# Optimization experiments

Measured on AMD Instinct MI355X. Metric: run time of the kernel, lower is better.

The kernel has to match this reference:

```python
import jax, jax.numpy as jnp
import numpy as np

INPUT_DIM = 256
NODE_DIM = 6
OUTPUT_DIM = 256
N_NODES = 10000
N_EDGES = 320000


def setup_inputs() -> dict:
    key = jax.random.key(0)
    ks = jax.random.split(key, 6)
    x = jax.random.normal(ks[0], (N_NODES, NODE_DIM), dtype=jnp.float32)
    edge_index = jax.random.randint(ks[1], (2, N_EDGES), 0, N_NODES, dtype=jnp.int64 if jax.config.jax_enable_x64 else jnp.int32)
    edge_attr = jax.random.normal(ks[2], (N_EDGES, INPUT_DIM), dtype=jnp.float32)
    mask = jax.random.uniform(ks[3], (N_EDGES,), dtype=jnp.float32)
    in_feat = INPUT_DIM * 3 + NODE_DIM * 2  # 774
    limit = float(np.sqrt(6.0 / (in_feat + OUTPUT_DIM)))  # xavier_uniform
    W = jax.random.uniform(ks[4], (OUTPUT_DIM, in_feat), dtype=jnp.float32, minval=-limit, maxval=limit)
    b = jax.random.uniform(ks[5], (OUTPUT_DIM,), dtype=jnp.float32, minval=-1.0 / np.sqrt(in_feat), maxval=1.0 / np.sqrt(in_feat))
    return {"x": x, "num_nodes": N_NODES, "edge_index": edge_index, "edge_attr": edge_attr, "mask": mask, "W": W, "b": b}


def reference(x, num_nodes, edge_index, edge_attr, mask, W, b):
    row = edge_index[0]
    col = edge_index[1]
    # masked mean-ish aggregation of edge features into destination nodes
    num = jax.ops.segment_sum(edge_attr * mask[:, None], col, num_segments=num_nodes)  # [N, input_dim]
    den = jax.ops.segment_sum(mask[:, None], col, num_segments=num_nodes)             # [N, 1]
    node_rep = num / (den + 1.0)
    node_rep = jnp.concatenate([node_rep, x], axis=1)  # [N, input_dim + node_dim]
    edge_rep = jnp.concatenate([node_rep[row], node_rep[col], edge_attr], axis=-1)  # [E, 3*input_dim + 2*node_dim]
    edge_rep = edge_rep @ W.T + b  # [E, output_dim]
    return (node_rep, edge_rep)
```

## Files before the change

### kernel.cpp

```cpp
#include <hip/hip_runtime.h>
#include <hip/hip_bf16.h>
#include <stdint.h>

typedef __attribute__((ext_vector_type(4))) float f32x4;
typedef __attribute__((ext_vector_type(8))) short bf16x8;

#define NDIM 6
#define IN_DIM 256
#define OUT_DIM 256
#define KW 780
#define NR 262
#define NRP 320
#define SCAN_T 1024

__device__ __forceinline__ short f2bf(float f) {
  return __builtin_bit_cast(short, __float2bfloat16(f));
}
__device__ __forceinline__ float bf2f(short h) {
  unsigned int u = ((unsigned int)(unsigned short)h) << 16;
  return __builtin_bit_cast(float, u);
}

__device__ __forceinline__ void gload_lds16(void* lds, const void* g) {
  __builtin_amdgcn_global_load_lds(
      (const __attribute__((address_space(1))) unsigned int*)g,
      (__attribute__((address_space(3))) unsigned int*)lds, 16, 0, 0);
}

__global__ void hist_kernel(const int* __restrict__ ei, int* __restrict__ counts, int E) {
  int e = blockIdx.x * 256 + threadIdx.x;
  if (e < E) atomicAdd(&counts[ei[(long)E + e]], 1);
}

__global__ __launch_bounds__(SCAN_T) void scan_kernel(const int* __restrict__ counts,
                                                      int* __restrict__ offsets, int N) {
  __shared__ int part[SCAN_T];
  int t = threadIdx.x;
  int chunk = (N + SCAN_T - 1) / SCAN_T;
  int begin = t * chunk;
  int s = 0;
  for (int i = 0; i < chunk; ++i) {
    int idx = begin + i;
    if (idx < N) s += counts[idx];
  }
  part[t] = s;
  __syncthreads();
  for (int d = 1; d < SCAN_T; d <<= 1) {
    int v = (t >= d) ? part[t - d] : 0;
    __syncthreads();
    part[t] += v;
    __syncthreads();
  }
  int run = (t == 0) ? 0 : part[t - 1];
  for (int i = 0; i < chunk; ++i) {
    int idx = begin + i;
    if (idx < N) { offsets[idx] = run; run += counts[idx]; }
  }
}

__global__ void scatter_kernel(const int* __restrict__ ei, const int* __restrict__ offsets,
                               int* __restrict__ cursor, int* __restrict__ csr, int E) {
  int e = blockIdx.x * 256 + threadIdx.x;
  if (e >= E) return;
  int col = ei[(long)E + e];
  int pos = atomicAdd(&cursor[col], 1);
  csr[offsets[col] + pos] = e;
}

__global__ __launch_bounds__(256) void reduce_kernel(
    const int* __restrict__ csr, const int* __restrict__ offsets,
    const int* __restrict__ counts, const float* __restrict__ ea,
    const float* __restrict__ mask, const float* __restrict__ x,
    float* __restrict__ outN, short* __restrict__ nrepb, int N) {
  int n = blockIdx.x * 4 + (threadIdx.x >> 6);
  if (n >= N) return;
  int lane = threadIdx.x & 63;
  int s = offsets[n], cnt = counts[n];
  f32x4 sum = (f32x4)0.0f;
  float den = 0.0f;

  int ecur = 0; float mcur = 0.0f;
  if (lane < cnt) { ecur = csr[s + lane]; mcur = mask[ecur]; }

  for (int base = 0; base < cnt; base += 64) {
    int enext = 0; float mnext = 0.0f;
    if (base + 64 < cnt) {
      int idx = base + 64 + lane;
      if (idx < cnt) { enext = csr[s + idx]; mnext = mask[enext]; }
    }
    int mbits = __builtin_bit_cast(int, mcur);
#pragma unroll
    for (int i = 0; i < 64; ++i) {
      if (base + i >= cnt) break;
      int e = __builtin_amdgcn_readlane(ecur, i);
      float m = __builtin_bit_cast(float, __builtin_amdgcn_readlane(mbits, i));
      f32x4 v = ((const f32x4*)ea)[(long)e * 64 + lane];
      sum.x += v.x * m; sum.y += v.y * m; sum.z += v.z * m; sum.w += v.w * m;
      den += m;
    }
    ecur = enext; mcur = mnext;
  }

  float inv = 1.0f / (den + 1.0f);
  sum.x *= inv; sum.y *= inv; sum.z *= inv; sum.w *= inv;
  float* po = outN + (long)n * NR + lane * 4;
  po[0] = sum.x; po[1] = sum.y; po[2] = sum.z; po[3] = sum.w;
  short4 pb;
  pb.x = f2bf(sum.x); pb.y = f2bf(sum.y); pb.z = f2bf(sum.z); pb.w = f2bf(sum.w);
  *(short4*)(nrepb + (long)n * NRP + lane * 4) = pb;
  if (lane < NDIM) {
    float xv = x[(long)n * NDIM + lane];
    outN[(long)n * NR + IN_DIM + lane] = xv;
    nrepb[(long)n * NRP + IN_DIM + lane] = f2bf(xv);
  } else if (lane < 8) {
    nrepb[(long)n * NRP + IN_DIM + lane] = 0;
  }
}

__global__ void wprep_kernel(const float* __restrict__ W, short* __restrict__ Weat,
                             short* __restrict__ Wrt, short* __restrict__ Wct) {
  int idx = blockIdx.x * 256 + threadIdx.x;
  if (idx < OUT_DIM * 256) {
    int n = idx >> 8, k = idx & 255;
    Weat[idx] = f2bf(W[(long)n * KW + 2 * NR + k]);
    return;
  }
  idx -= OUT_DIM * 256;
  if (idx < OUT_DIM * NRP) {
    int n = idx / NRP, k = idx % NRP;
    Wrt[idx] = f2bf(k < NR ? W[(long)n * KW + k] : 0.0f);
    return;
  }
  idx -= OUT_DIM * NRP;
  if (idx < OUT_DIM * NRP) {
    int n = idx / NRP, k = idx % NRP;
    Wct[idx] = f2bf(k < NR ? W[(long)n * KW + NR + k] : 0.0f);
  }
}

__global__ __launch_bounds__(256, 2) void pgemm_kernel(
    const short* __restrict__ nrepb, const short* __restrict__ Wrt,
    const short* __restrict__ Wct, const float* __restrict__ bias,
    short* __restrict__ Pr, short* __restrict__ Pc, int N) {
  __shared__ short As[5][64 * 64];
  const int tid = threadIdx.x;
  const int wave = tid >> 6, lane = tid & 63;
  const int m0 = blockIdx.x * 64;
  const int table = blockIdx.y;
  const short* Wt = table ? Wct : Wrt;
  short* P = table ? Pc : Pr;
  const int nbase = wave * 64;

  float bvals[4];
#pragma unroll
  for (int nf = 0; nf < 4; ++nf)
    bvals[nf] = table ? 0.0f : bias[nbase + 16 * nf + (lane & 15)];

  f32x4 acc[4][4];
#pragma unroll
  for (int mf = 0; mf < 4; ++mf)
#pragma unroll
    for (int nf = 0; nf < 4; ++nf) acc[mf][nf] = (f32x4)0.0f;

  bf16x8 bv[2][8];
  auto loadB = [&](int t, int tb) {
#pragma unroll
    for (int s2 = 0; s2 < 2; ++s2)
#pragma unroll
      for (int nf = 0; nf < 4; ++nf)
        bv[tb][s2 * 4 + nf] = *(const bf16x8*)&Wt[
            (long)(nbase + nf * 16 + (lane & 15)) * NRP + t * 64 + s2 * 32 + (lane >> 4) * 8];
  };

  const int scp = lane & 7;
#pragma unroll
  for (int t = 0; t < 5; ++t)
#pragma unroll
    for (int i = 0; i < 2; ++i) {
      int row = 16 * wave + 8 * i + (lane >> 3);
      int c = scp ^ (row & 7);
      long m = m0 + row; if (m >= N) m = N - 1;
      gload_lds16(&As[t][(16 * wave + 8 * i) * 64], nrepb + m * NRP + t * 64 + 8 * c);
    }
  loadB(0, 0);
  asm volatile("s_waitcnt vmcnt(8)" ::: "memory");
  __builtin_amdgcn_s_barrier();
  __builtin_amdgcn_sched_barrier(0);

#pragma unroll
  for (int t = 0; t < 5; ++t) {
    if (t < 4) loadB(t + 1, (t + 1) & 1);
    if (t < 4) asm volatile("s_waitcnt vmcnt(8)" ::: "memory");
    else       asm volatile("s_waitcnt vmcnt(0)" ::: "memory");
#pragma unroll
    for (int s2 = 0; s2 < 2; ++s2) {
      bf16x8 a[4];
      int cl = s2 * 4 + (lane >> 4);
#pragma unroll
      for (int mf = 0; mf < 4; ++mf) {
        int m = 16 * mf + (lane & 15);
        a[mf] = *(const bf16x8*)&As[t][m * 64 + ((cl ^ (m & 7)) * 8)];
      }
#pragma unroll
      for (int mf = 0; mf < 4; ++mf)
#pragma unroll
        for (int nf = 0; nf < 4; ++nf)
          acc[mf][nf] = __builtin_amdgcn_mfma_f32_16x16x32_bf16(
              a[mf], bv[t & 1][s2 * 4 + nf], acc[mf][nf], 0, 0, 0);
    }
  }

#pragma unroll
  for (int mf = 0; mf < 4; ++mf)
#pragma unroll
    for (int nf = 0; nf < 4; ++nf)
#pragma unroll
      for (int q = 0; q < 4; ++q) {
        long m = m0 + 16 * mf + (lane >> 4) * 4 + q;
        if (m < N)
          P[m * OUT_DIM + nbase + 16 * nf + (lane & 15)] = f2bf(acc[mf][nf][q] + bvals[nf]);
      }
}

__global__ __launch_bounds__(256, 2) void egemm_kernel(
    const int* __restrict__ ei, const float* __restrict__ ea,
    const short* __restrict__ Weat, const short* __restrict__ Pr,
    const short* __restrict__ Pc, float* __restrict__ outE, int E) {
  __shared__ short As[4][64 * 64];
  const int tid = threadIdx.x;
  const int wave = tid >> 6, lane = tid & 63;
  const long e0 = (long)blockIdx.x * 64;
  const int nbase = wave * 64;

  f32x4 acc[4][4];
#pragma unroll
  for (int mf = 0; mf < 4; ++mf)
#pragma unroll
    for (int nf = 0; nf < 4; ++nf) acc[mf][nf] = (f32x4)0.0f;

  bf16x8 bv[2][8];
  auto loadB = [&](int t, int tb) {
#pragma unroll
    for (int s2 = 0; s2 < 2; ++s2)
#pragma unroll
      for (int nf = 0; nf < 4; ++nf)
        bv[tb][s2 * 4 + nf] = *(const bf16x8*)&Weat[
            (nbase + nf * 16 + (lane & 15)) * 256 + t * 64 + s2 * 32 + (lane >> 4) * 8];
  };

  f32x4 eh[8][2];
#pragma unroll
  for (int j = 0; j < 8; ++j) {
    int c8 = tid + j * 256;
    int row = c8 >> 5, cp8 = c8 & 31;
    long e = e0 + row; if (e >= E) e = E - 1;
    const f32x4* s = (const f32x4*)(ea + (e * IN_DIM + cp8 * 8));
    eh[j][0] = s[0];
    eh[j][1] = s[1];
  }
  loadB(0, 0);
  __builtin_amdgcn_sched_barrier(0);
#pragma unroll
  for (int j = 0; j < 8; ++j) {
    int c8 = tid + j * 256;
    int row = c8 >> 5, cp8 = c8 & 31;
    int t = cp8 >> 3, cp = cp8 & 7;
    f32x4 v0 = eh[j][0], v1 = eh[j][1];
    bf16x8 p;
    p[0] = f2bf(v0.x); p[1] = f2bf(v0.y); p[2] = f2bf(v0.z); p[3] = f2bf(v0.w);
    p[4] = f2bf(v1.x); p[5] = f2bf(v1.y); p[6] = f2bf(v1.z); p[7] = f2bf(v1.w);
    *(bf16x8*)&As[t][row * 64 + ((cp ^ (row & 7)) * 8)] = p;
  }
  asm volatile("s_waitcnt lgkmcnt(0)" ::: "memory");
  __builtin_amdgcn_s_barrier();
  __builtin_amdgcn_sched_barrier(0);

#pragma unroll
  for (int t = 0; t < 4; ++t) {
    if (t < 3) loadB(t + 1, (t + 1) & 1);
    if (t < 3) asm volatile("s_waitcnt vmcnt(8)" ::: "memory");
    else       asm volatile("s_waitcnt vmcnt(0)" ::: "memory");
#pragma unroll
    for (int s2 = 0; s2 < 2; ++s2) {
      bf16x8 a[4];
      int cl = s2 * 4 + (lane >> 4);
#pragma unroll
      for (int mf = 0; mf < 4; ++mf) {
        int m = 16 * mf + (lane & 15);
        a[mf] = *(const bf16x8*)&As[t][m * 64 + ((cl ^ (m & 7)) * 8)];
      }
#pragma unroll
      for (int mf = 0; mf < 4; ++mf)
#pragma unroll
        for (int nf = 0; nf < 4; ++nf)
          acc[mf][nf] = __builtin_amdgcn_mfma_f32_16x16x32_bf16(
              a[mf], bv[t & 1][s2 * 4 + nf], acc[mf][nf], 0, 0, 0);
    }
  }

#pragma unroll
  for (int mf = 0; mf < 4; ++mf) {
#pragma unroll
    for (int q = 0; q < 4; ++q) {
      long e = e0 + 16 * mf + (lane >> 4) * 4 + q;
      bool ok = e < E;
      long ec = ok ? e : (E - 1);
      int re = ei[ec], ce = ei[(long)E + ec];
      const short* pr = Pr + (long)re * OUT_DIM;
      const short* pc = Pc + (long)ce * OUT_DIM;
      if (ok) {
#pragma unroll
        for (int nf = 0; nf < 4; ++nf) {
          int n = nbase + 16 * nf + (lane & 15);
          outE[e * OUT_DIM + n] = acc[mf][nf][q] + bf2f(pr[n]) + bf2f(pc[n]);
        }
      }
    }
  }
}

extern "C" void kernel_launch(void* const* d_in, const int* in_sizes, int n_in,
                              void* d_out, int out_size, void* d_ws, size_t ws_size,
                              hipStream_t stream) {
  const float* x    = (const float*)d_in[0];
  const int*   ei   = (const int*)d_in[2];
  const float* ea   = (const float*)d_in[3];
  const float* mask = (const float*)d_in[4];
  const float* W    = (const float*)d_in[5];
  const float* b    = (const float*)d_in[6];
  const int E = in_sizes[4];
  const int N = in_sizes[0] / NDIM;

  char* p = (char*)d_ws;
  int* counts  = (int*)p; p += (long)N * 4;
  int* cursor  = (int*)p; p += (long)N * 4;
  int* offsets = (int*)p; p += (long)(N + 1) * 4;
  int* csr     = (int*)p; p += (long)E * 4;
  p = (char*)(((uintptr_t)p + 15) & ~(uintptr_t)15);
  short* nrepb = (short*)p; p += (long)N * NRP * 2;
  short* Weat  = (short*)p; p += (long)OUT_DIM * 256 * 2;
  short* Wrt   = (short*)p; p += (long)OUT_DIM * NRP * 2;
  short* Wct   = (short*)p; p += (long)OUT_DIM * NRP * 2;
  short* Pr    = (short*)p; p += (long)N * OUT_DIM * 2;
  short* Pc    = (short*)p;

  float* outN = (float*)d_out;
  float* outE = outN + (long)N * NR;

  hipMemsetAsync(counts, 0, (size_t)2 * N * 4, stream);

  hist_kernel<<<(E + 255) / 256, 256, 0, stream>>>(ei, counts, E);
  scan_kernel<<<1, SCAN_T, 0, stream>>>(counts, offsets, N);
  scatter_kernel<<<(E + 255) / 256, 256, 0, stream>>>(ei, offsets, cursor, csr, E);
  reduce_kernel<<<(N + 3) / 4, 256, 0, stream>>>(csr, offsets, counts, ea, mask, x,
                                                 outN, nrepb, N);
  int wtot = OUT_DIM * 256 + 2 * OUT_DIM * NRP;
  wprep_kernel<<<(wtot + 255) / 256, 256, 0, stream>>>(W, Weat, Wrt, Wct);
  dim3 pg((N + 63) / 64, 2);
  pgemm_kernel<<<pg, 256, 0, stream>>>(nrepb, Wrt, Wct, b, Pr, Pc, N);
  egemm_kernel<<<(E + 63) / 64, 256, 0, stream>>>(ei, ea, Weat, Pr, Pc, outE, E);
}
```

Measured before the change: 383.9 us.

## Load edge_attr fragments directly from global into registers, dropping LDS staging

The edge GEMM kernel no longer stages the fp32 edge_attr tile through shared memory with a swizzled layout and barrier. Each wave now loads its A fragments straight from global memory, converts them to bf16 in registers, and loads W fragments per k-step. This removes the LDS writes and reads and the block barrier, and may let occupancy rise without the 32KB LDS footprint. In exchange, all four waves read the same A rows redundantly from global/L2, the loads are strided per lane, and the explicit B double-buffering with prefetch is gone.

Result: slower. 506.2 us (+31.9%).

```diff
diff --git a/kernel.cpp b/kernel.cpp
--- a/kernel.cpp
+++ b/kernel.cpp
@@ -226,83 +226,57 @@
     const int* __restrict__ ei, const float* __restrict__ ea,
     const short* __restrict__ Weat, const short* __restrict__ Pr,
     const short* __restrict__ Pc, float* __restrict__ outE, int E) {
-  __shared__ short As[4][64 * 64];
   const int tid = threadIdx.x;
   const int wave = tid >> 6, lane = tid & 63;
   const long e0 = (long)blockIdx.x * 64;
+  const int l15 = lane & 15, lg = lane >> 4;
   const int nbase = wave * 64;
 
+  const float* arow[4];
+#pragma unroll
+  for (int mf = 0; mf < 4; ++mf) {
+    long e = e0 + 16 * mf + l15; if (e >= E) e = E - 1;
+    arow[mf] = ea + e * IN_DIM + lg * 8;
+  }
+  const short* brow[4];
+#pragma unroll
+  for (int nf = 0; nf < 4; ++nf)
+    brow[nf] = Weat + (nbase + 16 * nf + l15) * 256 + lg * 8;
+
   f32x4 acc[4][4];
 #pragma unroll
   for (int mf = 0; mf < 4; ++mf)
 #pragma unroll
     for (int nf = 0; nf < 4; ++nf) acc[mf][nf] = (f32x4)0.0f;
 
-  bf16x8 bv[2][8];
-  auto loadB = [&](int t, int tb) {
-#pragma unroll
-    for (int s2 = 0; s2 < 2; ++s2)
+#pragma unroll
+  for (int ks = 0; ks < 8; ++ks) {
+    bf16x8 a[4], b[4];
+#pragma unroll
+    for (int mf = 0; mf < 4; ++mf) {
+      f32x4 v0 = *(const f32x4*)(arow[mf] + ks * 32);
+      f32x4 v1 = *(const f32x4*)(arow[mf] + ks * 32 + 4);
+      bf16x8 p;
+      p[0] = f2bf(v0.x); p[1] = f2bf(v0.y); p[2] = f2bf(v0.z); p[3] = f2bf(v0.w);
+      p[4] = f2bf(v1.x); p[5] = f2bf(v1.y); p[6] = f2bf(v1.z); p[7] = f2bf(v1.w);
+      a[mf] = p;
+    }
+#pragma unroll
+    for (int nf = 0; nf < 4; ++nf)
+      b[nf] = *(const bf16x8*)(brow[nf] + ks * 32);
+#pragma unroll
+    for (int mf = 0; mf < 4; ++mf)
 #pragma unroll
       for (int nf = 0; nf < 4; ++nf)
-        bv[tb][s2 * 4 + nf] = *(const bf16x8*)&Weat[
-            (nbase + nf * 16 + (lane & 15)) * 256 + t * 64 + s2 * 32 + (lane >> 4) * 8];
-  };
-
-  f32x4 eh[8][2];
-#pragma unroll
-  for (int j = 0; j < 8; ++j) {
-    int c8 = tid + j * 256;
-    int row = c8 >> 5, cp8 = c8 & 31;
-    long e = e0 + row; if (e >= E) e = E - 1;
-    const f32x4* s = (const f32x4*)(ea + (e * IN_DIM + cp8 * 8));
-    eh[j][0] = s[0];
-    eh[j][1] = s[1];
-  }
-  loadB(0, 0);
-  __builtin_amdgcn_sched_barrier(0);
-#pragma unroll
-  for (int j = 0; j < 8; ++j) {
-    int c8 = tid + j * 256;
-    int row = c8 >> 5, cp8 = c8 & 31;
-    int t = cp8 >> 3, cp = cp8 & 7;
-    f32x4 v0 = eh[j][0], v1 = eh[j][1];
-    bf16x8 p;
-    p[0] = f2bf(v0.x); p[1] = f2bf(v0.y); p[2] = f2bf(v0.z); p[3] = f2bf(v0.w);
-    p[4] = f2bf(v1.x); p[5] = f2bf(v1.y); p[6] = f2bf(v1.z); p[7] = f2bf(v1.w);
-    *(bf16x8*)&As[t][row * 64 + ((cp ^ (row & 7)) * 8)] = p;
-  }
-  asm volatile("s_waitcnt lgkmcnt(0)" ::: "memory");
-  __builtin_amdgcn_s_barrier();
-  __builtin_amdgcn_sched_barrier(0);
-
-#pragma unroll
-  for (int t = 0; t < 4; ++t) {
-    if (t < 3) loadB(t + 1, (t + 1) & 1);
-    if (t < 3) asm volatile("s_waitcnt vmcnt(8)" ::: "memory");
-    else       asm volatile("s_waitcnt vmcnt(0)" ::: "memory");
-#pragma unroll
-    for (int s2 = 0; s2 < 2; ++s2) {
-      bf16x8 a[4];
-      int cl = s2 * 4 + (lane >> 4);
-#pragma unroll
-      for (int mf = 0; mf < 4; ++mf) {
-        int m = 16 * mf + (lane & 15);
-        a[mf] = *(const bf16x8*)&As[t][m * 64 + ((cl ^ (m & 7)) * 8)];
-      }
-#pragma unroll
-      for (int mf = 0; mf < 4; ++mf)
-#pragma unroll
-        for (int nf = 0; nf < 4; ++nf)
-          acc[mf][nf] = __builtin_amdgcn_mfma_f32_16x16x32_bf16(
-              a[mf], bv[t & 1][s2 * 4 + nf], acc[mf][nf], 0, 0, 0);
-    }
+        acc[mf][nf] = __builtin_amdgcn_mfma_f32_16x16x32_bf16(
+            a[mf], b[nf], acc[mf][nf], 0, 0, 0);
   }
 
 #pragma unroll
   for (int mf = 0; mf < 4; ++mf) {
 #pragma unroll
     for (int q = 0; q < 4; ++q) {
-      long e = e0 + 16 * mf + (lane >> 4) * 4 + q;
+      long e = e0 + 16 * mf + lg * 4 + q;
       bool ok = e < E;
       long ec = ok ? e : (E - 1);
       int re = ei[ec], ce = ei[(long)E + ec];
@@ -311,7 +285,7 @@
       if (ok) {
 #pragma unroll
         for (int nf = 0; nf < 4; ++nf) {
-          int n = nbase + 16 * nf + (lane & 15);
+          int n = nbase + 16 * nf + l15;
           outE[e * OUT_DIM + n] = acc[mf][nf][q] + bf2f(pr[n]) + bf2f(pc[n]);
         }
       }
```

## Split edge GEMM output columns across two blocks and preload all weights

Applied to the files above, without the earlier changes.

The edge GEMM grid doubles so that each block computes 128 of the 256 output columns for its 64 edges, with each wave holding a 64x32 tile. All eight k-step weight fragments are loaded into registers up front instead of being double-buffered per stage, and MFMA issue is wrapped in s_setprio. Occupancy is raised to 3 blocks per SM. The cost is that every edge_attr row is now read from global memory and converted to bf16 twice, once per column half, and register pressure grows from holding all weight fragments at once.

After: 453.8 us. +18.2%, slower.

```diff
diff --git a/kernel.cpp b/kernel.cpp
--- a/kernel.cpp
+++ b/kernel.cpp
@@ -222,31 +222,23 @@
       }
 }
 
-__global__ __launch_bounds__(256, 2) void egemm_kernel(
+__global__ __launch_bounds__(256, 3) void egemm_kernel(
     const int* __restrict__ ei, const float* __restrict__ ea,
     const short* __restrict__ Weat, const short* __restrict__ Pr,
     const short* __restrict__ Pc, float* __restrict__ outE, int E) {
   __shared__ short As[4][64 * 64];
   const int tid = threadIdx.x;
   const int wave = tid >> 6, lane = tid & 63;
-  const long e0 = (long)blockIdx.x * 64;
-  const int nbase = wave * 64;
-
-  f32x4 acc[4][4];
+  const long e0 = (long)(blockIdx.x >> 1) * 64;
+  const int ch = blockIdx.x & 1;
+  const int l15 = lane & 15, lg = lane >> 4;
+  const int nbase = ch * 128 + wave * 32;
+
+  f32x4 acc[4][2];
 #pragma unroll
   for (int mf = 0; mf < 4; ++mf)
 #pragma unroll
-    for (int nf = 0; nf < 4; ++nf) acc[mf][nf] = (f32x4)0.0f;
-
-  bf16x8 bv[2][8];
-  auto loadB = [&](int t, int tb) {
-#pragma unroll
-    for (int s2 = 0; s2 < 2; ++s2)
-#pragma unroll
-      for (int nf = 0; nf < 4; ++nf)
-        bv[tb][s2 * 4 + nf] = *(const bf16x8*)&Weat[
-            (nbase + nf * 16 + (lane & 15)) * 256 + t * 64 + s2 * 32 + (lane >> 4) * 8];
-  };
+    for (int nf = 0; nf < 2; ++nf) acc[mf][nf] = (f32x4)0.0f;
 
   f32x4 eh[8][2];
 #pragma unroll
@@ -258,8 +250,15 @@
     eh[j][0] = s[0];
     eh[j][1] = s[1];
   }
-  loadB(0, 0);
+  bf16x8 bks[8][2];
+#pragma unroll
+  for (int ks = 0; ks < 8; ++ks)
+#pragma unroll
+    for (int nf = 0; nf < 2; ++nf)
+      bks[ks][nf] = *(const bf16x8*)&Weat[
+          (nbase + 16 * nf + l15) * 256 + ks * 32 + lg * 8];
   __builtin_amdgcn_sched_barrier(0);
+  asm volatile("s_waitcnt vmcnt(16)" ::: "memory");
 #pragma unroll
   for (int j = 0; j < 8; ++j) {
     int c8 = tid + j * 256;
@@ -271,38 +270,34 @@
     p[4] = f2bf(v1.x); p[5] = f2bf(v1.y); p[6] = f2bf(v1.z); p[7] = f2bf(v1.w);
     *(bf16x8*)&As[t][row * 64 + ((cp ^ (row & 7)) * 8)] = p;
   }
-  asm volatile("s_waitcnt lgkmcnt(0)" ::: "memory");
+  asm volatile("s_waitcnt vmcnt(0) lgkmcnt(0)" ::: "memory");
   __builtin_amdgcn_s_barrier();
   __builtin_amdgcn_sched_barrier(0);
 
 #pragma unroll
-  for (int t = 0; t < 4; ++t) {
-    if (t < 3) loadB(t + 1, (t + 1) & 1);
-    if (t < 3) asm volatile("s_waitcnt vmcnt(8)" ::: "memory");
-    else       asm volatile("s_waitcnt vmcnt(0)" ::: "memory");
-#pragma unroll
-    for (int s2 = 0; s2 < 2; ++s2) {
-      bf16x8 a[4];
-      int cl = s2 * 4 + (lane >> 4);
-#pragma unroll
-      for (int mf = 0; mf < 4; ++mf) {
-        int m = 16 * mf + (lane & 15);
-        a[mf] = *(const bf16x8*)&As[t][m * 64 + ((cl ^ (m & 7)) * 8)];
-      }
-#pragma unroll
-      for (int mf = 0; mf < 4; ++mf)
-#pragma unroll
-        for (int nf = 0; nf < 4; ++nf)
-          acc[mf][nf] = __builtin_amdgcn_mfma_f32_16x16x32_bf16(
-              a[mf], bv[t & 1][s2 * 4 + nf], acc[mf][nf], 0, 0, 0);
-    }
+  for (int ks = 0; ks < 8; ++ks) {
+    const int t = ks >> 1, cl = (ks & 1) * 4 + lg;
+    bf16x8 a[4];
+#pragma unroll
+    for (int mf = 0; mf < 4; ++mf) {
+      int m = 16 * mf + l15;
+      a[mf] = *(const bf16x8*)&As[t][m * 64 + ((cl ^ (m & 7)) * 8)];
+    }
+    __builtin_amdgcn_s_setprio(1);
+#pragma unroll
+    for (int mf = 0; mf < 4; ++mf)
+#pragma unroll
+      for (int nf = 0; nf < 2; ++nf)
+        acc[mf][nf] = __builtin_amdgcn_mfma_f32_16x16x32_bf16(
+            a[mf], bks[ks][nf], acc[mf][nf], 0, 0, 0);
+    __builtin_amdgcn_s_setprio(0);
   }
 
 #pragma unroll
   for (int mf = 0; mf < 4; ++mf) {
 #pragma unroll
     for (int q = 0; q < 4; ++q) {
-      long e = e0 + 16 * mf + (lane >> 4) * 4 + q;
+      long e = e0 + 16 * mf + lg * 4 + q;
       bool ok = e < E;
       long ec = ok ? e : (E - 1);
       int re = ei[ec], ce = ei[(long)E + ec];
@@ -310,8 +305,8 @@
       const short* pc = Pc + (long)ce * OUT_DIM;
       if (ok) {
 #pragma unroll
-        for (int nf = 0; nf < 4; ++nf) {
-          int n = nbase + 16 * nf + (lane & 15);
+        for (int nf = 0; nf < 2; ++nf) {
+          int n = nbase + 16 * nf + l15;
           outE[e * OUT_DIM + n] = acc[mf][nf][q] + bf2f(pr[n]) + bf2f(pc[n]);
         }
       }
@@ -358,5 +353,5 @@
   wprep_kernel<<<(wtot + 255) / 256, 256, 0, stream>>>(W, Weat, Wrt, Wct);
   dim3 pg((N + 63) / 64, 2);
   pgemm_kernel<<<pg, 256, 0, stream>>>(nrepb, Wrt, Wct, b, Pr, Pc, N);
-  egemm_kernel<<<(E + 63) / 64, 256, 0, stream>>>(ei, ea, Weat, Pr, Pc, outE, E);
-}
+  egemm_kernel<<<((E + 63) / 64) * 2, 256, 0, stream>>>(ei, ea, Weat, Pr, Pc, outE, E);
+}
```
